# Performance work log

Hardware: AMD Instinct MI355X
Metric: run time of the kernel (lower is better)

The kernel has to match this reference:

```python
import jax, jax.numpy as jnp
import numpy as np

D = 512
VOCAB = 8192
UTT_LEN = 16
BATCH = 32
NTYPES = 8
MPT = 32
NLAYERS = 2


def setup_inputs() -> dict:
    key = jax.random.key(0)
    ks = jax.random.split(key, 16)
    d, dff, v1 = D, 4 * D, VOCAB + 1
    s = 0.02
    nrm = lambda k, shape: jax.random.normal(k, shape, dtype=jnp.float32) * s
    zeros = lambda shape: jnp.zeros(shape, jnp.float32)
    ones = lambda shape: jnp.ones(shape, jnp.float32)
    return {
        'meanings': jax.random.randint(ks[0], (BATCH, NTYPES), 0, MPT),
        'emb_table': nrm(ks[1], (NTYPES * MPT, d)),
        'v2e_w': nrm(ks[2], (v1, d)),
        'e2v_w': nrm(ks[3], (v1, d)),
        'e2v_b': zeros((v1,)),
        'sa_qkv_w': nrm(ks[4], (NLAYERS, 3 * d, d)),
        'sa_qkv_b': zeros((NLAYERS, 3 * d)),
        'sa_out_w': nrm(ks[5], (NLAYERS, d, d)),
        'sa_out_b': zeros((NLAYERS, d)),
        'ca_qkv_w': nrm(ks[6], (NLAYERS, 3 * d, d)),
        'ca_qkv_b': zeros((NLAYERS, 3 * d)),
        'ca_out_w': nrm(ks[7], (NLAYERS, d, d)),
        'ca_out_b': zeros((NLAYERS, d)),
        'ffn_w1': nrm(ks[8], (NLAYERS, dff, d)),
        'ffn_b1': zeros((NLAYERS, dff)),
        'ffn_w2': nrm(ks[9], (NLAYERS, d, dff)),
        'ffn_b2': zeros((NLAYERS, d)),
        'ln1_g': ones((NLAYERS, d)), 'ln1_b': zeros((NLAYERS, d)),
        'ln2_g': ones((NLAYERS, d)), 'ln2_b': zeros((NLAYERS, d)),
        'ln3_g': ones((NLAYERS, d)), 'ln3_b': zeros((NLAYERS, d)),
    }


def _ln(x, g, b, eps=1e-5):
    m = x.mean(-1, keepdims=True)
    v = ((x - m) ** 2).mean(-1, keepdims=True)
    return (x - m) / jnp.sqrt(v + eps) * g + b


def _attn(q_in, kv_in, qkv_w, qkv_b, out_w, out_b, mask):
    # single-head attention, torch MultiheadAttention layout (seq, batch, d)
    d = q_in.shape[-1]
    q = q_in @ qkv_w[:d].T + qkv_b[:d]
    k = kv_in @ qkv_w[d:2 * d].T + qkv_b[d:2 * d]
    v = kv_in @ qkv_w[2 * d:].T + qkv_b[2 * d:]
    scores = jnp.einsum('qbd,kbd->bqk', q, k) / jnp.sqrt(jnp.float32(d))
    if mask is not None:
        scores = scores + mask
    a = jax.nn.softmax(scores, axis=-1)
    o = jnp.einsum('bqk,kbd->qbd', a, v)
    return o @ out_w.T + out_b


def _sinusoidal_pe(L, d):
    pos = np.arange(L)[:, None].astype(np.float32)
    div = np.exp(np.arange(0, d, 2).astype(np.float32) * (-np.log(10000.0) / d))
    pe = np.zeros((L, d), np.float32)
    pe[:, 0::2] = np.sin(pos * div)
    pe[:, 1::2] = np.cos(pos * div)
    return jnp.asarray(pe)[:, None, :]  # [L,1,d]


def reference(meanings, emb_table, v2e_w, e2v_w, e2v_b,
              sa_qkv_w, sa_qkv_b, sa_out_w, sa_out_b,
              ca_qkv_w, ca_qkv_b, ca_out_w, ca_out_b,
              ffn_w1, ffn_b1, ffn_w2, ffn_b2,
              ln1_g, ln1_b, ln2_g, ln2_b, ln3_g, ln3_b):
    B, T = meanings.shape
    v1, d = v2e_w.shape
    start_token = v1 - 1
    mpt = emb_table.shape[0] // T
    offs = jnp.arange(T, dtype=meanings.dtype) * mpt
    src = emb_table[meanings + offs].sum(axis=1)[None]  # [1,B,d] cross-attn memory
    L = UTT_LEN
    pe = _sinusoidal_pe(L, d)
    causal = jnp.where(jnp.tril(jnp.ones((L, L), bool)), 0.0, -jnp.inf).astype(jnp.float32)
    nlayers = sa_qkv_w.shape[0]

    def step(buf, i):
        # full-length decode with causal mask == original growing-prefix decode at position i
        x = v2e_w[buf[:L]] + pe  # [L,B,d]
        for l in range(nlayers):
            sa = _attn(x, x, sa_qkv_w[l], sa_qkv_b[l], sa_out_w[l], sa_out_b[l], causal)
            x = _ln(x + sa, ln1_g[l], ln1_b[l])
            ca = _attn(x, src, ca_qkv_w[l], ca_qkv_b[l], ca_out_w[l], ca_out_b[l], None)
            x = _ln(x + ca, ln2_g[l], ln2_b[l])
            ff = jax.nn.relu(x @ ffn_w1[l].T + ffn_b1[l]) @ ffn_w2[l].T + ffn_b2[l]
            x = _ln(x + ff, ln3_g[l], ln3_b[l])
        h = jnp.take(x, i, axis=0)         # [B,d] last generated position
        logits = h @ e2v_w.T + e2v_b        # [B,V+1]
        tok = jnp.argmax(logits, axis=-1).astype(buf.dtype)
        buf = buf.at[i + 1].set(tok)
        return buf, (tok, logits)

    buf0 = jnp.zeros((L + 1, B), jnp.int32).at[0].set(start_token)
    _, (toks, logits) = jax.lax.scan(step, buf0, jnp.arange(L))
    return toks, logits  # utterances [utt_len,B], per-step logits [utt_len,B,V+1]
```

## Files before the change

### kernel.cpp

```cpp
#include <hip/hip_runtime.h>
#include <cmath>

namespace {

constexpr int Dm  = 512;
constexpr int Bn  = 32;
constexpr int Lq  = 16;
constexpr int V1  = 8193;
constexpr int DFF = 2048;
constexpr int NL  = 2;
constexpr int NT  = 256;

__device__ __forceinline__ float wred(float v) {
#pragma unroll
  for (int off = 32; off; off >>= 1) v += __shfl_down(v, off, 64);
  return v;
}

__device__ __forceinline__ float dot4(const float4 w, const float4 x, float a) {
  a = fmaf(w.x, x.x, a); a = fmaf(w.y, x.y, a);
  a = fmaf(w.z, x.z, a); a = fmaf(w.w, x.w, a);
  return a;
}

__device__ __forceinline__ float pe_val(int pos, int t) {
  const int j2 = (t >> 1) << 1;
  const float div = expf((float)j2 * (-9.210340371976184f / 512.0f));
  const float ang = (float)pos * div;
  return (t & 1) ? cosf(ang) : sinf(ang);
}

template <int KS, int Kc, int SP, bool RELU>
__global__ __launch_bounds__(NT) void fg_part(
    const float* __restrict__ xsrc, int xstride, int srcPartStride,
    const float* __restrict__ W, int K,
    const float* __restrict__ bias,
    float* __restrict__ part, int N) {
  constexpr int QR = Kc / 4;
  __shared__ float smem[32 * Kc];
  const int kc = (int)blockIdx.x % KS;
  const int k0 = kc * Kc;
  for (int idx = threadIdx.x; idx < 8 * Kc; idx += NT) {
    const int b = idx / QR, q = idx - b * QR;
    const float* s0 = xsrc + (size_t)b * xstride + k0 + (q << 2);
    float4 v = *(const float4*)(s0);
#pragma unroll
    for (int s = 1; s < SP; ++s) {
      const float4 u = *(const float4*)(s0 + (size_t)s * srcPartStride);
      v.x += u.x; v.y += u.y; v.z += u.z; v.w += u.w;
    }
    if (RELU) {
      v.x = fmaxf(v.x, 0.f); v.y = fmaxf(v.y, 0.f);
      v.z = fmaxf(v.z, 0.f); v.w = fmaxf(v.w, 0.f);
    }
    *(float4*)(smem + b * Kc + ((q ^ (b & 7)) << 2)) = v;
  }
  __syncthreads();
  const int lane = (int)threadIdx.x & 63, wave = (int)threadIdx.x >> 6;
  const int bl = lane & 31, nh = lane >> 5, sw = bl & 7;
  const int rowjob = ((int)blockIdx.x / KS) * 4 + wave;
  const int n0 = (rowjob << 3) + (nh << 2);
  const float* xb = smem + bl * Kc;
  const float* w = W + (size_t)n0 * K + k0;
  float a0 = 0.f, a1 = 0.f, a2 = 0.f, a3 = 0.f;
#pragma unroll 4
  for (int qq = 0; qq < QR; ++qq) {
    const float4 xv = *(const float4*)(xb + ((qq ^ sw) << 2));
    const float* wq = w + (qq << 2);
    a0 = dot4(*(const float4*)(wq), xv, a0);
    a1 = dot4(*(const float4*)(wq + K), xv, a1);
    a2 = dot4(*(const float4*)(wq + 2 * K), xv, a2);
    a3 = dot4(*(const float4*)(wq + 3 * K), xv, a3);
  }
  if (kc == 0) {
    a0 += bias[n0]; a1 += bias[n0 + 1]; a2 += bias[n0 + 2]; a3 += bias[n0 + 3];
  }
  float* yb = part + (size_t)kc * 32 * N + (size_t)bl * N + n0;
  yb[0] = a0; yb[1] = a1; yb[2] = a2; yb[3] = a3;
}

__global__ __launch_bounds__(NT) void fg_qkv_part(const float* __restrict__ x,
    const float* __restrict__ W, const float* __restrict__ bias,
    float* __restrict__ qkvp) {
  constexpr int Kc = 128, QR = 32;
  __shared__ float smem[32 * Kc];
  const int kc = (int)blockIdx.x & 3;
  const int k0 = kc * Kc;
  for (int idx = threadIdx.x; idx < 8 * Kc; idx += NT) {
    const int b = idx / QR, q = idx - b * QR;
    const float4 v = *(const float4*)(x + (b << 9) + k0 + (q << 2));
    *(float4*)(smem + b * Kc + ((q ^ (b & 7)) << 2)) = v;
  }
  __syncthreads();
  const int lane = (int)threadIdx.x & 63, wave = (int)threadIdx.x >> 6;
  const int bl = lane & 31, nh = lane >> 5, sw = bl & 7;
  const int rowjob = ((int)blockIdx.x >> 2) * 4 + wave;
  const int n0 = (rowjob << 3) + (nh << 2);
  const float* xb = smem + bl * Kc;
  const float* w = W + (size_t)n0 * Dm + k0;
  float a0 = 0.f, a1 = 0.f, a2 = 0.f, a3 = 0.f;
#pragma unroll 4
  for (int qq = 0; qq < QR; ++qq) {
    const float4 xv = *(const float4*)(xb + ((qq ^ sw) << 2));
    const float* wq = w + (qq << 2);
    a0 = dot4(*(const float4*)(wq), xv, a0);
    a1 = dot4(*(const float4*)(wq + Dm), xv, a1);
    a2 = dot4(*(const float4*)(wq + 2 * Dm), xv, a2);
    a3 = dot4(*(const float4*)(wq + 3 * Dm), xv, a3);
  }
  if (kc == 0) {
    a0 += bias[n0]; a1 += bias[n0 + 1]; a2 += bias[n0 + 2]; a3 += bias[n0 + 3];
  }
  const int seg = n0 >> 9;
  float* yb = qkvp + (size_t)seg * 65536 + (size_t)kc * 16384 + (bl << 9) + (n0 & 511);
  yb[0] = a0; yb[1] = a1; yb[2] = a2; yb[3] = a3;
}

__device__ __forceinline__ void block_ln(float* s, const float* __restrict__ g,
                                         const float* __restrict__ bb, float* red) {
  const int tid = (int)threadIdx.x;
  float ls = 0.f, lq = 0.f;
  for (int t = tid; t < Dm; t += NT) { const float v = s[t]; ls += v; lq += v * v; }
  ls = wred(ls); lq = wred(lq);
  const int wave = tid >> 6, lane = tid & 63;
  if (lane == 0) { red[wave] = ls; red[4 + wave] = lq; }
  __syncthreads();
  const float sum = red[0] + red[1] + red[2] + red[3];
  const float sq  = red[4] + red[5] + red[6] + red[7];
  const float mean = sum * (1.f / Dm);
  const float var  = sq * (1.f / Dm) - mean * mean;
  const float inv  = 1.f / sqrtf(var + 1e-5f);
  __syncthreads();
  for (int t = tid; t < Dm; t += NT) s[t] = (s[t] - mean) * inv * g[t] + bb[t];
}

__global__ __launch_bounds__(NT) void attn_core(const float* __restrict__ qkvp,
    float* __restrict__ kcl, float* __restrict__ vcl,
    float* __restrict__ aout, int pos) {
  __shared__ float sQ[Dm], sK[Dm], sV[Dm], sS[Lq];
  const int b = blockIdx.x, tid = threadIdx.x, lane = tid & 63, wave = tid >> 6;
  const float* qp = qkvp;
  const float* kp = qkvp + 65536;
  const float* vp = qkvp + 131072;
  for (int t = tid; t < Dm; t += NT) {
    const int o = (b << 9) + t;
    const float qv = qp[o] + qp[o + 16384] + qp[o + 32768] + qp[o + 49152];
    const float kv = kp[o] + kp[o + 16384] + kp[o + 32768] + kp[o + 49152];
    const float vv = vp[o] + vp[o + 16384] + vp[o + 32768] + vp[o + 49152];
    sQ[t] = qv; sK[t] = kv; sV[t] = vv;
    const int co = ((pos * Bn + b) << 9) + t;
    kcl[co] = kv; vcl[co] = vv;
  }
  __syncthreads();
  for (int j = wave; j <= pos; j += 4) {
    float acc;
    if (j == pos) {
      acc = dot4(*(const float4*)(sK + (lane << 2)),
                 *(const float4*)(sQ + (lane << 2)), 0.f);
      acc = dot4(*(const float4*)(sK + 256 + (lane << 2)),
                 *(const float4*)(sQ + 256 + (lane << 2)), acc);
    } else {
      const float* kr = kcl + ((size_t)(j * Bn + b) << 9);
      acc = dot4(*(const float4*)(kr + (lane << 2)),
                 *(const float4*)(sQ + (lane << 2)), 0.f);
      acc = dot4(*(const float4*)(kr + 256 + (lane << 2)),
                 *(const float4*)(sQ + 256 + (lane << 2)), acc);
    }
    acc = wred(acc);
    if (lane == 0) sS[j] = acc * 0.044194173824159216f;
  }
  __syncthreads();
  if (tid == 0) {
    float m = -1e30f;
    for (int j = 0; j <= pos; ++j) m = fmaxf(m, sS[j]);
    float s = 0.f;
    for (int j = 0; j <= pos; ++j) { const float e = expf(sS[j] - m); sS[j] = e; s += e; }
    const float inv = 1.f / s;
    for (int j = 0; j <= pos; ++j) sS[j] *= inv;
  }
  __syncthreads();
  for (int t = tid; t < Dm; t += NT) {
    float acc = sS[pos] * sV[t];
    for (int j = 0; j < pos; ++j) acc += sS[j] * vcl[((size_t)(j * Bn + b) << 9) + t];
    aout[(b << 9) + t] = acc;
  }
}

__global__ __launch_bounds__(NT) void ln12(const float* __restrict__ sop,
    const float* __restrict__ caCp,
    const float* __restrict__ g1, const float* __restrict__ b1,
    const float* __restrict__ g2, const float* __restrict__ b2,
    float* __restrict__ x) {
  __shared__ float sR[Dm], red[8];
  const int b = blockIdx.x, tid = threadIdx.x;
  for (int t = tid; t < Dm; t += NT) {
    const int o = (b << 9) + t;
    sR[t] = x[o] + sop[o] + sop[o + 16384] + sop[o + 32768] + sop[o + 49152];
  }
  __syncthreads();
  block_ln(sR, g1, b1, red);
  __syncthreads();
  for (int t = tid; t < Dm; t += NT) {
    const int o = (b << 9) + t;
    sR[t] += caCp[o] + caCp[o + 16384] + caCp[o + 32768] + caCp[o + 49152];
  }
  __syncthreads();
  block_ln(sR, g2, b2, red);
  __syncthreads();
  for (int t = tid; t < Dm; t += NT) x[(b << 9) + t] = sR[t];
}

__global__ __launch_bounds__(NT) void ln3red(const float* __restrict__ f2p,
    const float* __restrict__ g3, const float* __restrict__ bb3,
    float* __restrict__ x) {
  __shared__ float sR[Dm], red[8];
  const int b = blockIdx.x, tid = threadIdx.x;
  for (int t = tid; t < Dm; t += NT) {
    const int o = (b << 9) + t;
    float v = x[o];
#pragma unroll
    for (int kc = 0; kc < 8; ++kc) v += f2p[kc * 16384 + o];
    sR[t] = v;
  }
  __syncthreads();
  block_ln(sR, g3, bb3, red);
  __syncthreads();
  for (int t = tid; t < Dm; t += NT) x[(b << 9) + t] = sR[t];
}

__global__ __launch_bounds__(512) void src_kernel(const int* __restrict__ meanings,
                                                  const float* __restrict__ emb,
                                                  float* __restrict__ src) {
  const int b = blockIdx.x, t = threadIdx.x;
  float s = 0.f;
#pragma unroll
  for (int ty = 0; ty < 8; ++ty) {
    const int idx = meanings[b * 8 + ty] + ty * 32;
    s += emb[(size_t)idx * Dm + t];
  }
  src[b * Dm + t] = s;
}

__global__ __launch_bounds__(512) void embed0(const float* __restrict__ v2e,
                                              float* __restrict__ x) {
  const int b = blockIdx.x, t = threadIdx.x;
  x[(b << 9) + t] = v2e[(size_t)(V1 - 1) * Dm + t] + pe_val(0, t);
}

__global__ __launch_bounds__(NT) void argmax_embed(float* __restrict__ x,
    const float* __restrict__ e2v_w, const float* __restrict__ e2v_b,
    const float* __restrict__ v2e, const float* __restrict__ lp,
    float* __restrict__ outLogits, float* __restrict__ outToks, int i) {
  __shared__ float red[8];
  __shared__ float sv[NT];
  __shared__ int   si[NT];
  const int b = blockIdx.x, tid = threadIdx.x, lane = tid & 63, wave = tid >> 6;
  float ls = 0.f;
  for (int t = tid; t < Dm; t += NT) ls += x[(b << 9) + t] * e2v_w[(size_t)8192 * Dm + t];
  ls = wred(ls);
  if (lane == 0) red[wave] = ls;
  __syncthreads();
  float* row = outLogits + ((size_t)i * Bn + b) * V1;
  if (tid == 0) {
    const float lg = red[0] + red[1] + red[2] + red[3] + e2v_b[8192];
    row[8192] = lg;
    red[4] = lg;
  }
  __syncthreads();
  const float lg = red[4];
  float best = -1e30f; int bi = 0;
  for (int v = tid; v < 8192; v += NT) {
    const float val = lp[(b << 13) + v] + lp[262144 + (b << 13) + v];
    row[v] = val;
    if (val > best) { best = val; bi = v; }
  }
  sv[tid] = best; si[tid] = bi;
  __syncthreads();
  for (int off = 128; off; off >>= 1) {
    if (tid < off) {
      const float v2 = sv[tid + off]; const int i2 = si[tid + off];
      if (v2 > sv[tid] || (v2 == sv[tid] && i2 < si[tid])) { sv[tid] = v2; si[tid] = i2; }
    }
    __syncthreads();
  }
  if (tid == 0) {
    int tok = si[0];
    if (lg > sv[0]) tok = 8192;
    outToks[i * Bn + b] = (float)tok;
    si[0] = tok;
  }
  __syncthreads();
  const int tok = si[0];
  if (i + 1 < Lq) {
    for (int t = tid; t < Dm; t += NT)
      x[(b << 9) + t] = v2e[(size_t)tok * Dm + t] + pe_val(i + 1, t);
  }
}

}

extern "C" void kernel_launch(void* const* d_in, const int* in_sizes, int n_in,
                              void* d_out, int out_size, void* d_ws, size_t ws_size,
                              hipStream_t stream) {
  (void)in_sizes; (void)n_in; (void)out_size; (void)ws_size;
  const int*   meanings  = (const int*)d_in[0];
  const float* emb_table = (const float*)d_in[1];
  const float* v2e_w     = (const float*)d_in[2];
  const float* e2v_w     = (const float*)d_in[3];
  const float* e2v_b     = (const float*)d_in[4];
  const float* sa_qkv_w  = (const float*)d_in[5];
  const float* sa_qkv_b  = (const float*)d_in[6];
  const float* sa_out_w  = (const float*)d_in[7];
  const float* sa_out_b  = (const float*)d_in[8];
  const float* ca_qkv_w  = (const float*)d_in[9];
  const float* ca_qkv_b  = (const float*)d_in[10];
  const float* ca_out_w  = (const float*)d_in[11];
  const float* ca_out_b  = (const float*)d_in[12];
  const float* ffn_w1    = (const float*)d_in[13];
  const float* ffn_b1    = (const float*)d_in[14];
  const float* ffn_w2    = (const float*)d_in[15];
  const float* ffn_b2    = (const float*)d_in[16];
  const float* ln1_g     = (const float*)d_in[17];
  const float* ln1_b     = (const float*)d_in[18];
  const float* ln2_g     = (const float*)d_in[19];
  const float* ln2_b     = (const float*)d_in[20];
  const float* ln3_g     = (const float*)d_in[21];
  const float* ln3_b     = (const float*)d_in[22];

  float* out = (float*)d_out;
  float* outLogits = out + Lq * Bn;

  float* f = (float*)d_ws;
  float* src  = f;  f += 16384;
  float* x    = f;  f += 16384;
  float* aout = f;  f += 16384;
  float* caCp = f;  f += 131072;
  float* regA = f;  f += 655360;
  float* kcache = f; f += 524288;
  float* vcache = f;
  float* qkvp = regA;
  float* sop  = regA + 196608;
  float* h1p  = regA + 262144;
  float* f2p  = regA + 524288;
  float* lp   = regA;

  src_kernel<<<Bn, 512, 0, stream>>>(meanings, emb_table, src);

  for (int l = 0; l < NL; ++l) {
    fg_part<4, 128, 1, false><<<64, NT, 0, stream>>>(src, Dm, 0,
        ca_qkv_w + ((size_t)l * 3 + 2) * Dm * Dm, Dm,
        ca_qkv_b + l * 3 * Dm + 2 * Dm, sop, Dm);
    fg_part<4, 128, 4, false><<<64, NT, 0, stream>>>(sop, Dm, 16384,
        ca_out_w + (size_t)l * Dm * Dm, Dm,
        ca_out_b + l * Dm, caCp + (size_t)l * 65536, Dm);
  }

  embed0<<<Bn, 512, 0, stream>>>(v2e_w, x);

  for (int i = 0; i < Lq; ++i) {
    for (int l = 0; l < NL; ++l) {
      float* kcl = kcache + (size_t)l * Lq * Bn * Dm;
      float* vcl = vcache + (size_t)l * Lq * Bn * Dm;
      fg_qkv_part<<<192, NT, 0, stream>>>(x,
          sa_qkv_w + (size_t)l * 3 * Dm * Dm, sa_qkv_b + l * 3 * Dm, qkvp);
      attn_core<<<Bn, NT, 0, stream>>>(qkvp, kcl, vcl, aout, i);
      fg_part<4, 128, 1, false><<<64, NT, 0, stream>>>(aout, Dm, 0,
          sa_out_w + (size_t)l * Dm * Dm, Dm, sa_out_b + l * Dm, sop, Dm);
      ln12<<<Bn, NT, 0, stream>>>(sop, caCp + (size_t)l * 65536,
          ln1_g + l * Dm, ln1_b + l * Dm, ln2_g + l * Dm, ln2_b + l * Dm, x);
      fg_part<4, 128, 1, false><<<256, NT, 0, stream>>>(x, Dm, 0,
          ffn_w1 + (size_t)l * DFF * Dm, Dm, ffn_b1 + l * DFF, h1p, DFF);
      fg_part<8, 256, 4, true><<<128, NT, 0, stream>>>(h1p, DFF, 65536,
          ffn_w2 + (size_t)l * Dm * DFF, DFF, ffn_b2 + l * Dm, f2p, Dm);
      ln3red<<<Bn, NT, 0, stream>>>(f2p,
          ln3_g + l * Dm, ln3_b + l * Dm, x);
    }
    fg_part<2, 256, 1, false><<<512, NT, 0, stream>>>(x, Dm, 0,
        e2v_w, Dm, e2v_b, lp, 8192);
    argmax_embed<<<Bn, NT, 0, stream>>>(x, e2v_w, e2v_b, v2e_w,
        lp, outLogits, out, i);
  }
}
```

Baseline: 2.736 ms.

## Fuse all decode phases into one persistent kernel with a sharded grid barrier

Replaces roughly 300 small kernel launches with one persistent kernel of 128 blocks. Phases are separated by a software grid barrier built from sharded atomic counters. Inter-phase data moves through relaxed agent-scope atomic loads and stores, and blocks loop over extra jobs where a phase has more than 128 jobs. This removes launch overhead and inter-kernel gaps, but it adds spin-wait barrier cost, loses parallelism in large phases such as the vocabulary projection (512 jobs on 128 blocks), and depends on all blocks being co-resident.

```diff
diff --git a/kernel.cpp b/kernel.cpp
--- a/kernel.cpp
+++ b/kernel.cpp
@@ -9,7 +9,53 @@
 constexpr int V1  = 8193;
 constexpr int DFF = 2048;
 constexpr int NL  = 2;
-constexpr int NT  = 256;
+
+constexpr int NB    = 128;
+constexpr int NT    = 256;
+constexpr int SHARD = 8;
+constexpr int SHSZ  = NB / SHARD;
+
+struct Params {
+  const int*   meanings;
+  const float* emb;
+  const float* v2e;
+  const float* e2v_w; const float* e2v_b;
+  const float* sa_qkv_w; const float* sa_qkv_b;
+  const float* sa_out_w; const float* sa_out_b;
+  const float* ca_qkv_w; const float* ca_qkv_b;
+  const float* ca_out_w; const float* ca_out_b;
+  const float* ffn_w1; const float* ffn_b1;
+  const float* ffn_w2; const float* ffn_b2;
+  const float* ln1_g; const float* ln1_b;
+  const float* ln2_g; const float* ln2_b;
+  const float* ln3_g; const float* ln3_b;
+  unsigned* bar;
+  float* src; float* x; float* aout; float* caCp;
+  float* qkvp; float* sop; float* h1p; float* f2p; float* lp;
+  float* kcache; float* vcache;
+  float* outToks; float* outLogits;
+};
+
+__device__ __forceinline__ float g_ld(const float* p) {
+  return __hip_atomic_load(p, __ATOMIC_RELAXED, __HIP_MEMORY_SCOPE_AGENT);
+}
+__device__ __forceinline__ void g_st(float* p, float v) {
+  __hip_atomic_store(p, v, __ATOMIC_RELAXED, __HIP_MEMORY_SCOPE_AGENT);
+}
+__device__ __forceinline__ float2 g_ld2(const float* p) {
+  unsigned long long u = __hip_atomic_load((const unsigned long long*)p,
+      __ATOMIC_RELAXED, __HIP_MEMORY_SCOPE_AGENT);
+  float2 r;
+  r.x = __uint_as_float((unsigned)u);
+  r.y = __uint_as_float((unsigned)(u >> 32));
+  return r;
+}
+__device__ __forceinline__ void g_st2(float* p, float a, float b) {
+  unsigned long long u = (unsigned long long)__float_as_uint(a) |
+                         ((unsigned long long)__float_as_uint(b) << 32);
+  __hip_atomic_store((unsigned long long*)p, u, __ATOMIC_RELAXED,
+                     __HIP_MEMORY_SCOPE_AGENT);
+}
 
 __device__ __forceinline__ float wred(float v) {
 #pragma unroll
@@ -30,94 +76,132 @@
   return (t & 1) ? cosf(ang) : sinf(ang);
 }
 
+__global__ __launch_bounds__(512) void init_bar(unsigned* bar) {
+  __hip_atomic_store(bar + threadIdx.x, 0u, __ATOMIC_RELAXED,
+                     __HIP_MEMORY_SCOPE_AGENT);
+}
+
+__device__ void gsync(unsigned* bar, unsigned& target) {
+  __syncthreads();
+  if (threadIdx.x == 0) {
+    asm volatile("" ::: "memory");
+    const unsigned old = __hip_atomic_fetch_add(
+        bar + (((unsigned)blockIdx.x & 7u) << 5), 1u,
+        __ATOMIC_RELEASE, __HIP_MEMORY_SCOPE_AGENT);
+    if (old == target * SHSZ - 1u) {
+      const unsigned mold = __hip_atomic_fetch_add(bar + 256, 1u,
+          __ATOMIC_RELAXED, __HIP_MEMORY_SCOPE_AGENT);
+      if (mold == target * SHARD - 1u) {
+        __hip_atomic_fetch_add(bar + 288, 1u, __ATOMIC_RELAXED,
+                               __HIP_MEMORY_SCOPE_AGENT);
+      }
+    }
+    while (__hip_atomic_load(bar + 288, __ATOMIC_RELAXED,
+                             __HIP_MEMORY_SCOPE_AGENT) < target) {
+      __builtin_amdgcn_s_sleep(1);
+    }
+    asm volatile("" ::: "memory");
+  }
+  __syncthreads();
+  ++target;
+}
+
 template <int KS, int Kc, int SP, bool RELU>
-__global__ __launch_bounds__(NT) void fg_part(
-    const float* __restrict__ xsrc, int xstride, int srcPartStride,
-    const float* __restrict__ W, int K,
-    const float* __restrict__ bias,
-    float* __restrict__ part, int N) {
+__device__ void ph_fg(float* smem, const float* __restrict__ xsrc, int xstride,
+                      int pstride, const float* __restrict__ W, int K,
+                      const float* __restrict__ bias,
+                      float* __restrict__ part, int N) {
+  const int bid = (int)blockIdx.x;
+  const int njobs = KS * (N >> 5);
+  if (bid >= njobs) return;
   constexpr int QR = Kc / 4;
-  __shared__ float smem[32 * Kc];
-  const int kc = (int)blockIdx.x % KS;
+  const int kc = bid % KS;
   const int k0 = kc * Kc;
   for (int idx = threadIdx.x; idx < 8 * Kc; idx += NT) {
     const int b = idx / QR, q = idx - b * QR;
     const float* s0 = xsrc + (size_t)b * xstride + k0 + (q << 2);
-    float4 v = *(const float4*)(s0);
+    float2 lo = g_ld2(s0), hi = g_ld2(s0 + 2);
 #pragma unroll
     for (int s = 1; s < SP; ++s) {
-      const float4 u = *(const float4*)(s0 + (size_t)s * srcPartStride);
-      v.x += u.x; v.y += u.y; v.z += u.z; v.w += u.w;
+      const float2 l2 = g_ld2(s0 + (size_t)s * pstride);
+      const float2 h2 = g_ld2(s0 + (size_t)s * pstride + 2);
+      lo.x += l2.x; lo.y += l2.y; hi.x += h2.x; hi.y += h2.y;
     }
     if (RELU) {
-      v.x = fmaxf(v.x, 0.f); v.y = fmaxf(v.y, 0.f);
-      v.z = fmaxf(v.z, 0.f); v.w = fmaxf(v.w, 0.f);
-    }
+      lo.x = fmaxf(lo.x, 0.f); lo.y = fmaxf(lo.y, 0.f);
+      hi.x = fmaxf(hi.x, 0.f); hi.y = fmaxf(hi.y, 0.f);
+    }
+    float4 v; v.x = lo.x; v.y = lo.y; v.z = hi.x; v.w = hi.y;
     *(float4*)(smem + b * Kc + ((q ^ (b & 7)) << 2)) = v;
   }
   __syncthreads();
   const int lane = (int)threadIdx.x & 63, wave = (int)threadIdx.x >> 6;
   const int bl = lane & 31, nh = lane >> 5, sw = bl & 7;
-  const int rowjob = ((int)blockIdx.x / KS) * 4 + wave;
-  const int n0 = (rowjob << 3) + (nh << 2);
   const float* xb = smem + bl * Kc;
-  const float* w = W + (size_t)n0 * K + k0;
-  float a0 = 0.f, a1 = 0.f, a2 = 0.f, a3 = 0.f;
+  for (int jid = bid; jid < njobs; jid += NB) {
+    const int rowjob = (jid / KS) * 4 + wave;
+    const int n0 = (rowjob << 3) + (nh << 2);
+    const float* w = W + (size_t)n0 * K + k0;
+    float a0 = 0.f, a1 = 0.f, a2 = 0.f, a3 = 0.f;
 #pragma unroll 4
-  for (int qq = 0; qq < QR; ++qq) {
-    const float4 xv = *(const float4*)(xb + ((qq ^ sw) << 2));
-    const float* wq = w + (qq << 2);
-    a0 = dot4(*(const float4*)(wq), xv, a0);
-    a1 = dot4(*(const float4*)(wq + K), xv, a1);
-    a2 = dot4(*(const float4*)(wq + 2 * K), xv, a2);
-    a3 = dot4(*(const float4*)(wq + 3 * K), xv, a3);
-  }
-  if (kc == 0) {
-    a0 += bias[n0]; a1 += bias[n0 + 1]; a2 += bias[n0 + 2]; a3 += bias[n0 + 3];
-  }
-  float* yb = part + (size_t)kc * 32 * N + (size_t)bl * N + n0;
-  yb[0] = a0; yb[1] = a1; yb[2] = a2; yb[3] = a3;
-}
-
-__global__ __launch_bounds__(NT) void fg_qkv_part(const float* __restrict__ x,
-    const float* __restrict__ W, const float* __restrict__ bias,
-    float* __restrict__ qkvp) {
+    for (int qq = 0; qq < QR; ++qq) {
+      const float4 xv = *(const float4*)(xb + ((qq ^ sw) << 2));
+      const float* wq = w + (qq << 2);
+      a0 = dot4(*(const float4*)(wq), xv, a0);
+      a1 = dot4(*(const float4*)(wq + K), xv, a1);
+      a2 = dot4(*(const float4*)(wq + 2 * K), xv, a2);
+      a3 = dot4(*(const float4*)(wq + 3 * K), xv, a3);
+    }
+    if (kc == 0) {
+      a0 += bias[n0]; a1 += bias[n0 + 1]; a2 += bias[n0 + 2]; a3 += bias[n0 + 3];
+    }
+    float* yb = part + (size_t)kc * 32 * N + (size_t)bl * N + n0;
+    g_st2(yb, a0, a1); g_st2(yb + 2, a2, a3);
+  }
+}
+
+__device__ void ph_qkv(float* smem, const float* __restrict__ x,
+                       const float* __restrict__ W, const float* __restrict__ bias,
+                       float* __restrict__ qkvp) {
   constexpr int Kc = 128, QR = 32;
-  __shared__ float smem[32 * Kc];
-  const int kc = (int)blockIdx.x & 3;
-  const int k0 = kc * Kc;
+  const int bid = (int)blockIdx.x;
+  const int kc = bid & 3, k0 = kc << 7;
   for (int idx = threadIdx.x; idx < 8 * Kc; idx += NT) {
     const int b = idx / QR, q = idx - b * QR;
-    const float4 v = *(const float4*)(x + (b << 9) + k0 + (q << 2));
+    const float* s0 = x + (b << 9) + k0 + (q << 2);
+    const float2 lo = g_ld2(s0), hi = g_ld2(s0 + 2);
+    float4 v; v.x = lo.x; v.y = lo.y; v.z = hi.x; v.w = hi.y;
     *(float4*)(smem + b * Kc + ((q ^ (b & 7)) << 2)) = v;
   }
   __syncthreads();
   const int lane = (int)threadIdx.x & 63, wave = (int)threadIdx.x >> 6;
   const int bl = lane & 31, nh = lane >> 5, sw = bl & 7;
-  const int rowjob = ((int)blockIdx.x >> 2) * 4 + wave;
-  const int n0 = (rowjob << 3) + (nh << 2);
   const float* xb = smem + bl * Kc;
-  const float* w = W + (size_t)n0 * Dm + k0;
-  float a0 = 0.f, a1 = 0.f, a2 = 0.f, a3 = 0.f;
+  for (int jid = bid; jid < 192; jid += NB) {
+    const int rowjob = (jid >> 2) * 4 + wave;
+    const int n0 = (rowjob << 3) + (nh << 2);
+    const float* w = W + (size_t)n0 * Dm + k0;
+    float a0 = 0.f, a1 = 0.f, a2 = 0.f, a3 = 0.f;
 #pragma unroll 4
-  for (int qq = 0; qq < QR; ++qq) {
-    const float4 xv = *(const float4*)(xb + ((qq ^ sw) << 2));
-    const float* wq = w + (qq << 2);
-    a0 = dot4(*(const float4*)(wq), xv, a0);
-    a1 = dot4(*(const float4*)(wq + Dm), xv, a1);
-    a2 = dot4(*(const float4*)(wq + 2 * Dm), xv, a2);
-    a3 = dot4(*(const float4*)(wq + 3 * Dm), xv, a3);
-  }
-  if (kc == 0) {
-    a0 += bias[n0]; a1 += bias[n0 + 1]; a2 += bias[n0 + 2]; a3 += bias[n0 + 3];
-  }
-  const int seg = n0 >> 9;
-  float* yb = qkvp + (size_t)seg * 65536 + (size_t)kc * 16384 + (bl << 9) + (n0 & 511);
-  yb[0] = a0; yb[1] = a1; yb[2] = a2; yb[3] = a3;
-}
-
-__device__ __forceinline__ void block_ln(float* s, const float* __restrict__ g,
-                                         const float* __restrict__ bb, float* red) {
+    for (int qq = 0; qq < QR; ++qq) {
+      const float4 xv = *(const float4*)(xb + ((qq ^ sw) << 2));
+      const float* wq = w + (qq << 2);
+      a0 = dot4(*(const float4*)(wq), xv, a0);
+      a1 = dot4(*(const float4*)(wq + Dm), xv, a1);
+      a2 = dot4(*(const float4*)(wq + 2 * Dm), xv, a2);
+      a3 = dot4(*(const float4*)(wq + 3 * Dm), xv, a3);
+    }
+    if (kc == 0) {
+      a0 += bias[n0]; a1 += bias[n0 + 1]; a2 += bias[n0 + 2]; a3 += bias[n0 + 3];
+    }
+    const int seg = n0 >> 9;
+    float* yb = qkvp + (size_t)seg * 65536 + (size_t)kc * 16384 + (bl << 9) + (n0 & 511);
+    g_st2(yb, a0, a1); g_st2(yb + 2, a2, a3);
+  }
+}
+
+__device__ void block_ln(float* s, const float* __restrict__ g,
+                         const float* __restrict__ bb, float* red) {
   const int tid = (int)threadIdx.x;
   float ls = 0.f, lq = 0.f;
   for (int t = tid; t < Dm; t += NT) { const float v = s[t]; ls += v; lq += v * v; }
@@ -134,19 +218,21 @@
   for (int t = tid; t < Dm; t += NT) s[t] = (s[t] - mean) * inv * g[t] + bb[t];
 }
 
-__global__ __launch_bounds__(NT) void attn_core(const float* __restrict__ qkvp,
-    float* __restrict__ kcl, float* __restrict__ vcl,
-    float* __restrict__ aout, int pos) {
-  __shared__ float sQ[Dm], sK[Dm], sV[Dm], sS[Lq];
-  const int b = blockIdx.x, tid = threadIdx.x, lane = tid & 63, wave = tid >> 6;
+__device__ void ph_attn(float* smem, const float* __restrict__ qkvp,
+                        float* __restrict__ kcl, float* __restrict__ vcl,
+                        float* __restrict__ aout, int pos) {
+  const int b = (int)blockIdx.x, tid = (int)threadIdx.x;
+  const int lane = tid & 63, wave = tid >> 6;
+  float* sQ = smem; float* sK = smem + 512; float* sV = smem + 1024;
+  float* sS = smem + 1536;
   const float* qp = qkvp;
   const float* kp = qkvp + 65536;
   const float* vp = qkvp + 131072;
   for (int t = tid; t < Dm; t += NT) {
     const int o = (b << 9) + t;
-    const float qv = qp[o] + qp[o + 16384] + qp[o + 32768] + qp[o + 49152];
-    const float kv = kp[o] + kp[o + 16384] + kp[o + 32768] + kp[o + 49152];
-    const float vv = vp[o] + vp[o + 16384] + vp[o + 32768] + vp[o + 49152];
+    const float qv = g_ld(qp + o) + g_ld(qp + o + 16384) + g_ld(qp + o + 32768) + g_ld(qp + o + 49152);
+    const float kv = g_ld(kp + o) + g_ld(kp + o + 16384) + g_ld(kp + o + 32768) + g_ld(kp + o + 49152);
+    const float vv = g_ld(vp + o) + g_ld(vp + o + 16384) + g_ld(vp + o + 32768) + g_ld(vp + o + 49152);
     sQ[t] = qv; sK[t] = kv; sV[t] = vv;
     const int co = ((pos * Bn + b) << 9) + t;
     kcl[co] = kv; vcl[co] = vv;
@@ -182,97 +268,105 @@
   for (int t = tid; t < Dm; t += NT) {
     float acc = sS[pos] * sV[t];
     for (int j = 0; j < pos; ++j) acc += sS[j] * vcl[((size_t)(j * Bn + b) << 9) + t];
-    aout[(b << 9) + t] = acc;
-  }
-}
-
-__global__ __launch_bounds__(NT) void ln12(const float* __restrict__ sop,
-    const float* __restrict__ caCp,
-    const float* __restrict__ g1, const float* __restrict__ b1,
-    const float* __restrict__ g2, const float* __restrict__ b2,
-    float* __restrict__ x) {
-  __shared__ float sR[Dm], red[8];
-  const int b = blockIdx.x, tid = threadIdx.x;
+    g_st(aout + (b << 9) + t, acc);
+  }
+}
+
+__device__ void ph_ln12(float* smem, const float* __restrict__ sop,
+                        const float* __restrict__ caCp,
+                        const float* __restrict__ g1, const float* __restrict__ b1,
+                        const float* __restrict__ g2, const float* __restrict__ b2,
+                        float* __restrict__ x) {
+  const int b = (int)blockIdx.x, tid = (int)threadIdx.x;
+  float* sR = smem; float* red = smem + 512;
   for (int t = tid; t < Dm; t += NT) {
     const int o = (b << 9) + t;
-    sR[t] = x[o] + sop[o] + sop[o + 16384] + sop[o + 32768] + sop[o + 49152];
+    sR[t] = g_ld(x + o) + g_ld(sop + o) + g_ld(sop + o + 16384) +
+            g_ld(sop + o + 32768) + g_ld(sop + o + 49152);
   }
   __syncthreads();
   block_ln(sR, g1, b1, red);
   __syncthreads();
   for (int t = tid; t < Dm; t += NT) {
     const int o = (b << 9) + t;
-    sR[t] += caCp[o] + caCp[o + 16384] + caCp[o + 32768] + caCp[o + 49152];
+    sR[t] += g_ld(caCp + o) + g_ld(caCp + o + 16384) +
+             g_ld(caCp + o + 32768) + g_ld(caCp + o + 49152);
   }
   __syncthreads();
   block_ln(sR, g2, b2, red);
   __syncthreads();
-  for (int t = tid; t < Dm; t += NT) x[(b << 9) + t] = sR[t];
-}
-
-__global__ __launch_bounds__(NT) void ln3red(const float* __restrict__ f2p,
-    const float* __restrict__ g3, const float* __restrict__ bb3,
-    float* __restrict__ x) {
-  __shared__ float sR[Dm], red[8];
-  const int b = blockIdx.x, tid = threadIdx.x;
+  for (int t = tid; t < Dm; t += NT) g_st(x + (b << 9) + t, sR[t]);
+}
+
+__device__ void ph_ln3(float* smem, const float* __restrict__ f2p,
+                       const float* __restrict__ g3, const float* __restrict__ bb3,
+                       float* __restrict__ x) {
+  const int b = (int)blockIdx.x, tid = (int)threadIdx.x;
+  float* sR = smem; float* red = smem + 512;
   for (int t = tid; t < Dm; t += NT) {
     const int o = (b << 9) + t;
-    float v = x[o];
+    float v = g_ld(x + o);
 #pragma unroll
-    for (int kc = 0; kc < 8; ++kc) v += f2p[kc * 16384 + o];
+    for (int kc = 0; kc < 8; ++kc) v += g_ld(f2p + kc * 16384 + o);
     sR[t] = v;
   }
   __syncthreads();
   block_ln(sR, g3, bb3, red);
   __syncthreads();
-  for (int t = tid; t < Dm; t += NT) x[(b << 9) + t] = sR[t];
-}
-
-__global__ __launch_bounds__(512) void src_kernel(const int* __restrict__ meanings,
-                                                  const float* __restrict__ emb,
-                                                  float* __restrict__ src) {
-  const int b = blockIdx.x, t = threadIdx.x;
-  float s = 0.f;
+  for (int t = tid; t < Dm; t += NT) g_st(x + (b << 9) + t, sR[t]);
+}
+
+__device__ void ph_src(const int* __restrict__ meanings,
+                       const float* __restrict__ emb, float* __restrict__ src) {
+  const int b = (int)blockIdx.x;
+  int m[8];
 #pragma unroll
-  for (int ty = 0; ty < 8; ++ty) {
-    const int idx = meanings[b * 8 + ty] + ty * 32;
-    s += emb[(size_t)idx * Dm + t];
-  }
-  src[b * Dm + t] = s;
-}
-
-__global__ __launch_bounds__(512) void embed0(const float* __restrict__ v2e,
-                                              float* __restrict__ x) {
-  const int b = blockIdx.x, t = threadIdx.x;
-  x[(b << 9) + t] = v2e[(size_t)(V1 - 1) * Dm + t] + pe_val(0, t);
-}
-
-__global__ __launch_bounds__(NT) void argmax_embed(float* __restrict__ x,
-    const float* __restrict__ e2v_w, const float* __restrict__ e2v_b,
-    const float* __restrict__ v2e, const float* __restrict__ lp,
-    float* __restrict__ outLogits, float* __restrict__ outToks, int i) {
-  __shared__ float red[8];
-  __shared__ float sv[NT];
-  __shared__ int   si[NT];
-  const int b = blockIdx.x, tid = threadIdx.x, lane = tid & 63, wave = tid >> 6;
+  for (int ty = 0; ty < 8; ++ty) m[ty] = meanings[b * 8 + ty] + ty * 32;
+  for (int t = (int)threadIdx.x; t < Dm; t += NT) {
+    float s = 0.f;
+#pragma unroll
+    for (int ty = 0; ty < 8; ++ty) s += emb[(size_t)m[ty] * Dm + t];
+    g_st(src + b * Dm + t, s);
+  }
+}
+
+__device__ void ph_embed0(const float* __restrict__ v2e, float* __restrict__ x, int b) {
+  for (int t = (int)threadIdx.x; t < Dm; t += NT)
+    g_st(x + (b << 9) + t, v2e[(size_t)(V1 - 1) * Dm + t] + pe_val(0, t));
+}
+
+__device__ void ph_argmax(float* smem, float* __restrict__ x,
+                          const float* __restrict__ e2v_w, const float* __restrict__ e2v_b,
+                          const float* __restrict__ v2e, const float* __restrict__ lp,
+                          float* __restrict__ outLogits, float* __restrict__ outToks,
+                          int i) {
+  const int b = (int)blockIdx.x, tid = (int)threadIdx.x;
+  const int lane = tid & 63, wave = tid >> 6;
+  float* red = smem;
+  float* sv  = smem + 8;
+  int*   si  = (int*)(smem + 8 + NT);
   float ls = 0.f;
-  for (int t = tid; t < Dm; t += NT) ls += x[(b << 9) + t] * e2v_w[(size_t)8192 * Dm + t];
+  for (int t = tid; t < Dm; t += NT)
+    ls += g_ld(x + (b << 9) + t) * e2v_w[(size_t)8192 * Dm + t];
   ls = wred(ls);
   if (lane == 0) red[wave] = ls;
   __syncthreads();
   float* row = outLogits + ((size_t)i * Bn + b) * V1;
   if (tid == 0) {
     const float lg = red[0] + red[1] + red[2] + red[3] + e2v_b[8192];
-    row[8192] = lg;
+    g_st(row + 8192, lg);
     red[4] = lg;
   }
   __syncthreads();
   const float lg = red[4];
   float best = -1e30f; int bi = 0;
-  for (int v = tid; v < 8192; v += NT) {
-    const float val = lp[(b << 13) + v] + lp[262144 + (b << 13) + v];
-    row[v] = val;
-    if (val > best) { best = val; bi = v; }
+  for (int v0 = tid * 2; v0 < 8192; v0 += NT * 2) {
+    const float2 a = g_ld2(lp + (b << 13) + v0);
+    const float2 c = g_ld2(lp + 262144 + (b << 13) + v0);
+    const float va = a.x + c.x, vb = a.y + c.y;
+    g_st(row + v0, va); g_st(row + v0 + 1, vb);
+    if (va > best) { best = va; bi = v0; }
+    if (vb > best) { best = vb; bi = v0 + 1; }
   }
   sv[tid] = best; si[tid] = bi;
   __syncthreads();
@@ -286,14 +380,66 @@
   if (tid == 0) {
     int tok = si[0];
     if (lg > sv[0]) tok = 8192;
-    outToks[i * Bn + b] = (float)tok;
+    g_st(outToks + i * Bn + b, (float)tok);
     si[0] = tok;
   }
   __syncthreads();
   const int tok = si[0];
   if (i + 1 < Lq) {
     for (int t = tid; t < Dm; t += NT)
-      x[(b << 9) + t] = v2e[(size_t)tok * Dm + t] + pe_val(i + 1, t);
+      g_st(x + (b << 9) + t, v2e[(size_t)tok * Dm + t] + pe_val(i + 1, t));
+  }
+}
+
+__global__ __launch_bounds__(NT) void persist(Params p) {
+  __shared__ float smem[8192];
+  const int bid = (int)blockIdx.x;
+  unsigned target = 1;
+
+  if (bid < Bn) ph_src(p.meanings, p.emb, p.src);
+  gsync(p.bar, target);
+
+  for (int l = 0; l < NL; ++l) {
+    ph_fg<4, 128, 1, false>(smem, p.src, Dm, 0,
+        p.ca_qkv_w + ((size_t)l * 3 + 2) * Dm * Dm, Dm,
+        p.ca_qkv_b + l * 3 * Dm + 2 * Dm, p.sop, Dm);
+    gsync(p.bar, target);
+    ph_fg<4, 128, 4, false>(smem, p.sop, Dm, 16384,
+        p.ca_out_w + (size_t)l * Dm * Dm, Dm,
+        p.ca_out_b + l * Dm, p.caCp + (size_t)l * 65536, Dm);
+    if (l == 0 && bid >= 64 && bid < 96) ph_embed0(p.v2e, p.x, bid - 64);
+    gsync(p.bar, target);
+  }
+
+  for (int i = 0; i < Lq; ++i) {
+    for (int l = 0; l < NL; ++l) {
+      float* kcl = p.kcache + (size_t)l * Lq * Bn * Dm;
+      float* vcl = p.vcache + (size_t)l * Lq * Bn * Dm;
+      ph_qkv(smem, p.x, p.sa_qkv_w + (size_t)l * 3 * Dm * Dm,
+             p.sa_qkv_b + l * 3 * Dm, p.qkvp);
+      gsync(p.bar, target);
+      if (bid < Bn) ph_attn(smem, p.qkvp, kcl, vcl, p.aout, i);
+      gsync(p.bar, target);
+      ph_fg<4, 128, 1, false>(smem, p.aout, Dm, 0,
+          p.sa_out_w + (size_t)l * Dm * Dm, Dm, p.sa_out_b + l * Dm, p.sop, Dm);
+      gsync(p.bar, target);
+      if (bid < Bn) ph_ln12(smem, p.sop, p.caCp + (size_t)l * 65536,
+          p.ln1_g + l * Dm, p.ln1_b + l * Dm, p.ln2_g + l * Dm, p.ln2_b + l * Dm, p.x);
+      gsync(p.bar, target);
+      ph_fg<4, 128, 1, false>(smem, p.x, Dm, 0,
+          p.ffn_w1 + (size_t)l * DFF * Dm, Dm, p.ffn_b1 + l * DFF, p.h1p, DFF);
+      gsync(p.bar, target);
+      ph_fg<8, 256, 4, true>(smem, p.h1p, DFF, 65536,
+          p.ffn_w2 + (size_t)l * Dm * DFF, DFF, p.ffn_b2 + l * Dm, p.f2p, Dm);
+      gsync(p.bar, target);
+      if (bid < Bn) ph_ln3(smem, p.f2p, p.ln3_g + l * Dm, p.ln3_b + l * Dm, p.x);
+      gsync(p.bar, target);
+    }
+    ph_fg<2, 256, 1, false>(smem, p.x, Dm, 0, p.e2v_w, Dm, p.e2v_b, p.lp, 8192);
+    gsync(p.bar, target);
+    if (bid < Bn) ph_argmax(smem, p.x, p.e2v_w, p.e2v_b, p.v2e, p.lp,
+                            p.outLogits, p.outToks, i);
+    gsync(p.bar, target);
   }
 }
 
@@ -303,81 +449,48 @@
                               void* d_out, int out_size, void* d_ws, size_t ws_size,
                               hipStream_t stream) {
   (void)in_sizes; (void)n_in; (void)out_size; (void)ws_size;
-  const int*   meanings  = (const int*)d_in[0];
-  const float* emb_table = (const float*)d_in[1];
-  const float* v2e_w     = (const float*)d_in[2];
-  const float* e2v_w     = (const float*)d_in[3];
-  const float* e2v_b     = (const float*)d_in[4];
-  const float* sa_qkv_w  = (const float*)d_in[5];
-  const float* sa_qkv_b  = (const float*)d_in[6];
-  const float* sa_out_w  = (const float*)d_in[7];
-  const float* sa_out_b  = (const float*)d_in[8];
-  const float* ca_qkv_w  = (const float*)d_in[9];
-  const float* ca_qkv_b  = (const float*)d_in[10];
-  const float* ca_out_w  = (const float*)d_in[11];
-  const float* ca_out_b  = (const float*)d_in[12];
-  const float* ffn_w1    = (const float*)d_in[13];
-  const float* ffn_b1    = (const float*)d_in[14];
-  const float* ffn_w2    = (const float*)d_in[15];
-  const float* ffn_b2    = (const float*)d_in[16];
-  const float* ln1_g     = (const float*)d_in[17];
-  const float* ln1_b     = (const float*)d_in[18];
-  const float* ln2_g     = (const float*)d_in[19];
-  const float* ln2_b     = (const float*)d_in[20];
-  const float* ln3_g     = (const float*)d_in[21];
-  const float* ln3_b     = (const float*)d_in[22];
-
-  float* out = (float*)d_out;
-  float* outLogits = out + Lq * Bn;
-
-  float* f = (float*)d_ws;
-  float* src  = f;  f += 16384;
-  float* x    = f;  f += 16384;
-  float* aout = f;  f += 16384;
-  float* caCp = f;  f += 131072;
+  char* ws = (char*)d_ws;
+
+  Params p;
+  p.meanings = (const int*)d_in[0];
+  p.emb      = (const float*)d_in[1];
+  p.v2e      = (const float*)d_in[2];
+  p.e2v_w    = (const float*)d_in[3];
+  p.e2v_b    = (const float*)d_in[4];
+  p.sa_qkv_w = (const float*)d_in[5];
+  p.sa_qkv_b = (const float*)d_in[6];
+  p.sa_out_w = (const float*)d_in[7];
+  p.sa_out_b = (const float*)d_in[8];
+  p.ca_qkv_w = (const float*)d_in[9];
+  p.ca_qkv_b = (const float*)d_in[10];
+  p.ca_out_w = (const float*)d_in[11];
+  p.ca_out_b = (const float*)d_in[12];
+  p.ffn_w1   = (const float*)d_in[13];
+  p.ffn_b1   = (const float*)d_in[14];
+  p.ffn_w2   = (const float*)d_in[15];
+  p.ffn_b2   = (const float*)d_in[16];
+  p.ln1_g = (const float*)d_in[17]; p.ln1_b = (const float*)d_in[18];
+  p.ln2_g = (const float*)d_in[19]; p.ln2_b = (const float*)d_in[20];
+  p.ln3_g = (const float*)d_in[21]; p.ln3_b = (const float*)d_in[22];
+
+  p.bar = (unsigned*)ws;
+  float* f = (float*)(ws + 4096);
+  p.src  = f;  f += 16384;
+  p.x    = f;  f += 16384;
+  p.aout = f;  f += 16384;
+  p.caCp = f;  f += 131072;
   float* regA = f;  f += 655360;
-  float* kcache = f; f += 524288;
-  float* vcache = f;
-  float* qkvp = regA;
-  float* sop  = regA + 196608;
-  float* h1p  = regA + 262144;
-  float* f2p  = regA + 524288;
-  float* lp   = regA;
-
-  src_kernel<<<Bn, 512, 0, stream>>>(meanings, emb_table, src);
-
-  for (int l = 0; l < NL; ++l) {
-    fg_part<4, 128, 1, false><<<64, NT, 0, stream>>>(src, Dm, 0,
-        ca_qkv_w + ((size_t)l * 3 + 2) * Dm * Dm, Dm,
-        ca_qkv_b + l * 3 * Dm + 2 * Dm, sop, Dm);
-    fg_part<4, 128, 4, false><<<64, NT, 0, stream>>>(sop, Dm, 16384,
-        ca_out_w + (size_t)l * Dm * Dm, Dm,
-        ca_out_b + l * Dm, caCp + (size_t)l * 65536, Dm);
-  }
-
-  embed0<<<Bn, 512, 0, stream>>>(v2e_w, x);
-
-  for (int i = 0; i < Lq; ++i) {
-    for (int l = 0; l < NL; ++l) {
-      float* kcl = kcache + (size_t)l * Lq * Bn * Dm;
-      float* vcl = vcache + (size_t)l * Lq * Bn * Dm;
-      fg_qkv_part<<<192, NT, 0, stream>>>(x,
-          sa_qkv_w + (size_t)l * 3 * Dm * Dm, sa_qkv_b + l * 3 * Dm, qkvp);
-      attn_core<<<Bn, NT, 0, stream>>>(qkvp, kcl, vcl, aout, i);
-      fg_part<4, 128, 1, false><<<64, NT, 0, stream>>>(aout, Dm, 0,
-          sa_out_w + (size_t)l * Dm * Dm, Dm, sa_out_b + l * Dm, sop, Dm);
-      ln12<<<Bn, NT, 0, stream>>>(sop, caCp + (size_t)l * 65536,
-          ln1_g + l * Dm, ln1_b + l * Dm, ln2_g + l * Dm, ln2_b + l * Dm, x);
-      fg_part<4, 128, 1, false><<<256, NT, 0, stream>>>(x, Dm, 0,
-          ffn_w1 + (size_t)l * DFF * Dm, Dm, ffn_b1 + l * DFF, h1p, DFF);
-      fg_part<8, 256, 4, true><<<128, NT, 0, stream>>>(h1p, DFF, 65536,
-          ffn_w2 + (size_t)l * Dm * DFF, DFF, ffn_b2 + l * Dm, f2p, Dm);
-      ln3red<<<Bn, NT, 0, stream>>>(f2p,
-          ln3_g + l * Dm, ln3_b + l * Dm, x);
-    }
-    fg_part<2, 256, 1, false><<<512, NT, 0, stream>>>(x, Dm, 0,
-        e2v_w, Dm, e2v_b, lp, 8192);
-    argmax_embed<<<Bn, NT, 0, stream>>>(x, e2v_w, e2v_b, v2e_w,
-        lp, outLogits, out, i);
-  }
-}
+  p.kcache = f; f += 524288;
+  p.vcache = f;
+  p.qkvp = regA;
+  p.sop  = regA + 196608;
+  p.h1p  = regA + 262144;
+  p.f2p  = regA + 524288;
+  p.lp   = regA;
+
+  p.outToks   = (float*)d_out;
+  p.outLogits = (float*)d_out + Lq * Bn;
+
+  init_bar<<<1, 512, 0, stream>>>(p.bar);
+  persist<<<NB, NT, 0, stream>>>(p);
+}
```

Result: slower. 4.009 ms (+46.5%).
